# Optimization experiments

Measured on AMD Instinct MI355X. Metric: run time of the kernel, lower is better.

The kernel has to match this reference:

```python
import jax, jax.numpy as jnp
import numpy as np

D_MODEL = 1024
HEADDIM = 64
EXPAND = 2
D_STATE = 128
D_CONV = 4
NGROUPS = 1
D_INNER = EXPAND * D_MODEL            # 2048
NHEADS = D_INNER // HEADDIM           # 32
CONV_DIM = D_INNER + 2 * NGROUPS * D_STATE
D_IN_PROJ = 2 * D_INNER + 2 * NGROUPS * D_STATE + NHEADS
BATCH = 2
SEQLEN = 1024
EPS = 1e-5


def silu(v):
    return v * jax.nn.sigmoid(v)


def setup_inputs() -> dict:
    key = jax.random.key(0)
    ks = jax.random.split(key, 8)
    s = 0.02
    return {
        "x": jax.random.normal(ks[0], (BATCH, SEQLEN, D_MODEL), jnp.float32),
        "in_proj_w": jax.random.normal(ks[1], (D_IN_PROJ, D_MODEL), jnp.float32) * s,
        "conv_w": jax.random.normal(ks[2], (CONV_DIM, D_CONV), jnp.float32) * 0.2,
        "conv_b": jax.random.normal(ks[3], (CONV_DIM,), jnp.float32) * 0.02,
        "dt_bias": jax.random.normal(ks[4], (NHEADS,), jnp.float32) * 0.1,
        "A_log": jax.random.normal(ks[5], (NHEADS,), jnp.float32) * 0.5,
        "D": jax.random.normal(ks[6], (NHEADS,), jnp.float32) * 0.5,
        "norm_w": jnp.ones((D_INNER,), jnp.float32),
        "out_proj_w": jax.random.normal(ks[7], (D_MODEL, D_INNER), jnp.float32) * s,
    }


def _mamba2(x, in_proj_w, conv_w, conv_b, dt_bias, A_log, D, norm_w, out_proj_w):
    b, l, _ = x.shape
    # input projection -> z | xBC | dt
    zxbcdt = x @ in_proj_w.T                                  # [b,l,d_in_proj]
    z, xBC, dt = jnp.split(zxbcdt, [D_INNER, D_INNER + CONV_DIM], axis=-1)
    dt = jax.nn.softplus(dt + dt_bias)                        # [b,l,nh]
    # causal depthwise conv over time, then SiLU
    rhs = conv_w.T[:, None, :]                                # [d_conv, 1, conv_dim]
    xBC = jax.lax.conv_general_dilated(
        xBC, rhs, window_strides=(1,), padding=[(D_CONV - 1, 0)],
        dimension_numbers=("NWC", "WIO", "NWC"), feature_group_count=CONV_DIM)
    xBC = silu(xBC + conv_b)
    xs, Bm, Cm = jnp.split(xBC, [D_INNER, D_INNER + D_STATE], axis=-1)
    xs = xs.reshape(b, l, NHEADS, HEADDIM)                    # [b,l,h,p]
    A = -jnp.exp(A_log)                                       # [nh], negative
    dA = jnp.exp(dt * A)                                      # [b,l,nh] in (0,1)
    # selective scan: h_t = dA_t * h_{t-1} + dt_t * x_t (outer) B_t; y_t = h_t C_t
    def step(h, inp):
        dA_t, x_t, B_t, dt_t, C_t = inp                       # [b,h],[b,h,p],[b,n],[b,h],[b,n]
        h = h * dA_t[:, :, None, None] + jnp.einsum("bh,bhp,bn->bhpn", dt_t, x_t, B_t)
        y = jnp.einsum("bhpn,bn->bhp", h, C_t)
        return h, y

    h0 = jnp.zeros((b, NHEADS, HEADDIM, D_STATE), x.dtype)
    xs_t = xs.transpose(1, 0, 2, 3)
    _, ys = jax.lax.scan(step, h0, (dA.transpose(1, 0, 2), xs_t,
                                    Bm.transpose(1, 0, 2), dt.transpose(1, 0, 2),
                                    Cm.transpose(1, 0, 2)))
    y = ys.transpose(1, 0, 2, 3) + D[None, None, :, None] * xs  # skip term
    y = y.reshape(b, l, D_INNER)
    # gated RMSNorm (norm_before_gate=False): rmsnorm(y * silu(z)) * w
    y = y * silu(z)
    y = y * jax.lax.rsqrt(jnp.mean(y * y, axis=-1, keepdims=True) + EPS) * norm_w
    return y @ out_proj_w.T


def reference(x, in_proj_w, conv_w, conv_b, dt_bias, A_log, D, norm_w, out_proj_w):
    return x + _mamba2(x, in_proj_w, conv_w, conv_b, dt_bias, A_log, D, norm_w, out_proj_w)
```

## Files before the change

kernel.cpp:

```cpp
#include <hip/hip_runtime.h>
#include <hip/hip_bf16.h>
#include <math.h>

#define NHEADS   32
#define CONV_DIM 2304
#define D_INNER  2048
#define SEQLEN   1024
#define NROWS    2048
#define ZX_STR   4352
#define D_MODEL  1024
#define Q        64
#define NCHUNK   16
#define XT_STR   72

typedef __attribute__((ext_vector_type(8))) short bhalf8;
typedef __attribute__((ext_vector_type(8))) short short8;
typedef __attribute__((ext_vector_type(4))) short short4v;
typedef __attribute__((ext_vector_type(4))) float f32x4;

__device__ __forceinline__ float bf2f(__hip_bfloat16 v){ return __bfloat162float(v); }
__device__ __forceinline__ short f2bs(float f){ __hip_bfloat16 h = __float2bfloat16(f); return *(short*)&h; }
__device__ __forceinline__ float s2f(short s){ __hip_bfloat16 h = *(__hip_bfloat16*)&s; return __bfloat162float(h); }
__device__ __forceinline__ float rdin(const void* p, size_t i, int isf){
    return isf ? ((const float*)p)[i] : __bfloat162float(((const __hip_bfloat16*)p)[i]);
}

__global__ __launch_bounds__(256)
void detect_dtype(const unsigned short* __restrict__ p, int* __restrict__ flag)
{
    int cnt = 0;
    for (int i = threadIdx.x; i < 4096; i += 256) {
        unsigned short u = p[2 * i];
        int e = (u >> 7) & 0xFF;
        cnt += (e >= 90 && e <= 141) ? 1 : 0;
    }
#pragma unroll
    for (int m = 1; m < 64; m <<= 1) cnt += __shfl_xor(cnt, m);
    __shared__ int red[4];
    if ((threadIdx.x & 63) == 0) red[threadIdx.x >> 6] = cnt;
    __syncthreads();
    if (threadIdx.x == 0) *flag = ((red[0]+red[1]+red[2]+red[3]) < 2048) ? 1 : 0;
}

#define XN8 262144
#define WN8 561152
#define ON8 262144
__global__ __launch_bounds__(256)
void to_bf16_all(const void* __restrict__ xs, const void* __restrict__ ws,
                 const void* __restrict__ os,
                 __hip_bfloat16* __restrict__ xd, __hip_bfloat16* __restrict__ wd,
                 __hip_bfloat16* __restrict__ od, const int* __restrict__ flagp)
{
    const int isf = *flagp;
    int i = blockIdx.x * 256 + threadIdx.x;
    const void* src; __hip_bfloat16* dst; int j;
    if (i < XN8)            { src = xs; dst = xd; j = i; }
    else if (i < XN8 + WN8) { src = ws; dst = wd; j = i - XN8; }
    else                    { src = os; dst = od; j = i - XN8 - WN8; }
    if (isf) {
        const float4* s = (const float4*)src;
        float4 a = s[2 * j], b = s[2 * j + 1];
        short8 r;
        r[0]=f2bs(a.x); r[1]=f2bs(a.y); r[2]=f2bs(a.z); r[3]=f2bs(a.w);
        r[4]=f2bs(b.x); r[5]=f2bs(b.y); r[6]=f2bs(b.z); r[7]=f2bs(b.w);
        ((short8*)dst)[j] = r;
    } else {
        ((float4*)dst)[j] = ((const float4*)src)[j];
    }
}

template<int MODE, int MT, int NT, int WROWS, int WCOLS>
__global__ __launch_bounds__(256)
void gemm_bt(const __hip_bfloat16* __restrict__ A,
             const __hip_bfloat16* __restrict__ W,
             __hip_bfloat16* __restrict__ Cb,
             const void* __restrict__ xraw,
             void* __restrict__ outv,
             const int* __restrict__ flagp,
             int K, int N)
{
    constexpr int FM = MT / WROWS / 16;
    constexpr int FN = NT / WCOLS / 16;
    constexpr int AI = MT / 32;
    constexpr int BI = NT / 32;
    __shared__ short As[MT * 64];
    __shared__ short Bs[NT * 64];
    const int m0 = blockIdx.y * MT;
    const int n0 = blockIdx.x * NT;
    const int wave = threadIdx.x >> 6;
    const int lane = threadIdx.x & 63;
    const int lr8 = lane >> 3, lc8 = lane & 7;
    const int lr  = lane & 15, lq  = lane >> 4;
    const int wm = (wave / WCOLS) * (MT / WROWS);
    const int wn = (wave % WCOLS) * (NT / WCOLS);

    f32x4 acc[FM][FN];
#pragma unroll
    for (int i = 0; i < FM; ++i)
#pragma unroll
        for (int j = 0; j < FN; ++j) acc[i][j] = (f32x4){0.f,0.f,0.f,0.f};

    for (int k0 = 0; k0 < K; k0 += 64) {
#pragma unroll
        for (int i = 0; i < AI; ++i) {
            const int rt = (wave * AI + i) * 8;
            const __hip_bfloat16* gp = A + (size_t)(m0 + rt + lr8) * K + k0 + lc8 * 8;
            __builtin_amdgcn_global_load_lds(
                (const __attribute__((address_space(1))) void*)gp,
                (__attribute__((address_space(3))) void*)&As[rt * 64], 16, 0, 0);
        }
#pragma unroll
        for (int i = 0; i < BI; ++i) {
            const int rt = (wave * BI + i) * 8;
            const __hip_bfloat16* gp = W + (size_t)(n0 + rt + lr8) * K + k0 + lc8 * 8;
            __builtin_amdgcn_global_load_lds(
                (const __attribute__((address_space(1))) void*)gp,
                (__attribute__((address_space(3))) void*)&Bs[rt * 64], 16, 0, 0);
        }
        __syncthreads();
#pragma unroll
        for (int kk = 0; kk < 64; kk += 32) {
            bhalf8 af[FM], bfv[FN];
#pragma unroll
            for (int t = 0; t < FM; ++t)
                af[t]  = *(const bhalf8*)&As[(wm + t * 16 + lr) * 64 + kk + lq * 8];
#pragma unroll
            for (int t = 0; t < FN; ++t)
                bfv[t] = *(const bhalf8*)&Bs[(wn + t * 16 + lr) * 64 + kk + lq * 8];
#pragma unroll
            for (int ti = 0; ti < FM; ++ti)
#pragma unroll
                for (int tj = 0; tj < FN; ++tj)
                    acc[ti][tj] = __builtin_amdgcn_mfma_f32_16x16x32_bf16(
                        af[ti], bfv[tj], acc[ti][tj], 0, 0, 0);
        }
        __syncthreads();
    }

    const int isf = (MODE == 1) ? *flagp : 0;
#pragma unroll
    for (int ti = 0; ti < FM; ++ti)
#pragma unroll
        for (int tj = 0; tj < FN; ++tj)
#pragma unroll
            for (int r = 0; r < 4; ++r) {
                int m = m0 + wm + ti * 16 + lq * 4 + r;
                int n = n0 + wn + tj * 16 + lr;
                size_t idx = (size_t)m * N + n;
                float v = acc[ti][tj][r];
                if (MODE == 0) {
                    Cb[idx] = __float2bfloat16(v);
                } else {
                    v += rdin(xraw, idx, isf);
                    if (isf) ((float*)outv)[idx] = v;
                    else     ((__hip_bfloat16*)outv)[idx] = __float2bfloat16(v);
                }
            }
}

__global__ __launch_bounds__(256)
void dt_kernel(const void* __restrict__ xraw, const void* __restrict__ wraw,
               const void* __restrict__ dt_bias,
               const int* __restrict__ flagp,
               float* __restrict__ dtp)
{
    const int isf = *flagp;
    const int row = blockIdx.x;
    __shared__ float xs[D_MODEL];
    for (int k = threadIdx.x; k < D_MODEL; k += 256)
        xs[k] = rdin(xraw, (size_t)row * D_MODEL + k, isf);
    __syncthreads();
    const int h = threadIdx.x >> 3;
    const int t = threadIdx.x & 7;
    const size_t wbase = (size_t)(4352 + h) * D_MODEL;
    float s = 0.f;
    for (int k = t; k < D_MODEL; k += 8)
        s += xs[k] * rdin(wraw, wbase + k, isf);
    s += __shfl_xor(s, 1);
    s += __shfl_xor(s, 2);
    s += __shfl_xor(s, 4);
    if (t == 0) {
        float raw = s + rdin(dt_bias, h, isf);
        dtp[(size_t)row * NHEADS + h] = raw > 20.f ? raw : log1pf(expf(raw));
    }
}

__global__ __launch_bounds__(256)
void conv_silu(const __hip_bfloat16* __restrict__ zxb,
               const void* __restrict__ conv_w, const void* __restrict__ conv_b,
               const int* __restrict__ flagp,
               __hip_bfloat16* __restrict__ xs_bf,
               __hip_bfloat16* __restrict__ B_bf,
               __hip_bfloat16* __restrict__ C_bf)
{
    const int isf = *flagp;
    const int row = blockIdx.x;
    const int l = row & (SEQLEN - 1);
    for (int c = threadIdx.x; c < CONV_DIM; c += 256) {
        float acc = rdin(conv_b, c, isf);
#pragma unroll
        for (int j = 0; j < 4; ++j) {
            int ls = l - 3 + j;
            if (ls >= 0)
                acc += bf2f(zxb[(size_t)(row - 3 + j) * ZX_STR + 2048 + c]) *
                       rdin(conv_w, (size_t)c * 4 + j, isf);
        }
        float v = acc / (1.f + expf(-acc));
        __hip_bfloat16 bv = __float2bfloat16(v);
        if (c < 2048)       xs_bf[(size_t)row * 2048 + c] = bv;
        else if (c < 2176)  B_bf[(size_t)row * 128 + (c - 2048)] = bv;
        else                C_bf[(size_t)row * 128 + (c - 2176)] = bv;
    }
}

__global__ __launch_bounds__(256)
void chunk_kernel(const __hip_bfloat16* __restrict__ xs_bf,
                  const __hip_bfloat16* __restrict__ B_bf,
                  const __hip_bfloat16* __restrict__ C_bf,
                  const float* __restrict__ dtp, const void* __restrict__ Alog,
                  const int* __restrict__ flagp,
                  float* __restrict__ cumg, float* __restrict__ decayg,
                  __hip_bfloat16* __restrict__ M_bf, float* __restrict__ S)
{
    __shared__ float cumS[Q], uS[Q], dtS[Q];
    __shared__ short Xt[64 * XT_STR];
    __shared__ short Bt[128 * XT_STR];
    const int bhc = blockIdx.x;
    const int c = bhc & 15, h = (bhc >> 4) & 31, b = bhc >> 9;
    const int row0 = b * SEQLEN + c * Q;
    const int isf = *flagp;

    if (threadIdx.x < 64) {
        const int t = threadIdx.x;
        const float An = -expf(rdin(Alog, h, isf));
        const float dt = dtp[(size_t)(row0 + t) * NHEADS + h];
        float cum = dt * An;
#pragma unroll
        for (int ofs = 1; ofs < 64; ofs <<= 1) {
            float v = __shfl_up(cum, ofs);
            if (t >= ofs) cum += v;
        }
        float tot = __shfl(cum, 63);
        cumS[t] = cum; dtS[t] = dt;
        uS[t] = expf(tot - cum) * dt;
        cumg[(size_t)bhc * Q + t] = cum;
        if (t == 63) decayg[bhc] = expf(tot);
    }
    __syncthreads();

#pragma unroll
    for (int i = 0; i < 2; ++i) {
        int seg = threadIdx.x + i * 256;
        int t = seg >> 3, p8 = (seg & 7) * 8;
        float ut = uS[t];
        bhalf8 v = *(const bhalf8*)&xs_bf[(size_t)(row0 + t) * 2048 + h * 64 + p8];
#pragma unroll
        for (int j = 0; j < 8; ++j)
            Xt[(p8 + j) * XT_STR + t] = f2bs(s2f(v[j]) * ut);
    }
#pragma unroll
    for (int i = 0; i < 4; ++i) {
        int seg = threadIdx.x + i * 256;
        int t = seg >> 4, n8 = (seg & 15) * 8;
        bhalf8 v = *(const bhalf8*)&B_bf[(size_t)(row0 + t) * 128 + n8];
#pragma unroll
        for (int j = 0; j < 8; ++j)
            Bt[(n8 + j) * XT_STR + t] = v[j];
    }

    const int wave = threadIdx.x >> 6, lane = threadIdx.x & 63;
    const int lr = lane & 15, lq = lane >> 4;

    {
        const int t0 = wave * 16;
        f32x4 acc[4];
#pragma unroll
        for (int j = 0; j < 4; ++j) acc[j] = (f32x4){0.f,0.f,0.f,0.f};
#pragma unroll
        for (int kk = 0; kk < 128; kk += 32) {
            bhalf8 af = *(const bhalf8*)&C_bf[(size_t)(row0 + t0 + lr) * 128 + kk + lq * 8];
#pragma unroll
            for (int j = 0; j < 4; ++j) {
                bhalf8 bf = *(const bhalf8*)&B_bf[(size_t)(row0 + j * 16 + lr) * 128 + kk + lq * 8];
                acc[j] = __builtin_amdgcn_mfma_f32_16x16x32_bf16(af, bf, acc[j], 0, 0, 0);
            }
        }
#pragma unroll
        for (int j = 0; j < 4; ++j)
#pragma unroll
            for (int r = 0; r < 4; ++r) {
                int t = t0 + lq * 4 + r;
                int s = j * 16 + lr;
                float m = (s <= t) ? acc[j][r] * expf(cumS[t] - cumS[s]) * dtS[s] : 0.f;
                M_bf[(size_t)bhc * 4096 + t * 64 + s] = __float2bfloat16(m);
            }
    }
    __syncthreads();

    {
        const int p0 = wave * 16;
        f32x4 acc[8];
#pragma unroll
        for (int j = 0; j < 8; ++j) acc[j] = (f32x4){0.f,0.f,0.f,0.f};
#pragma unroll
        for (int kk = 0; kk < 64; kk += 32) {
            bhalf8 af = *(const bhalf8*)&Xt[(p0 + lr) * XT_STR + kk + lq * 8];
#pragma unroll
            for (int j = 0; j < 8; ++j) {
                bhalf8 bf = *(const bhalf8*)&Bt[(j * 16 + lr) * XT_STR + kk + lq * 8];
                acc[j] = __builtin_amdgcn_mfma_f32_16x16x32_bf16(af, bf, acc[j], 0, 0, 0);
            }
        }
#pragma unroll
        for (int j = 0; j < 8; ++j)
#pragma unroll
            for (int r = 0; r < 4; ++r) {
                int p = p0 + lq * 4 + r;
                int n = j * 16 + lr;
                S[(size_t)bhc * 8192 + p * 128 + n] = acc[j][r];
            }
    }
}

__global__ __launch_bounds__(256)
void rec_kernel(const float* __restrict__ S, const float* __restrict__ decayg,
                __hip_bfloat16* __restrict__ hst)
{
    const int bh = blockIdx.x >> 3;
    const int sl = blockIdx.x & 7;
    const int off = sl * 1024 + threadIdx.x * 4;
    float h0 = 0.f, h1 = 0.f, h2 = 0.f, h3 = 0.f;
    for (int c = 0; c < NCHUNK; ++c) {
        size_t base = ((size_t)bh * NCHUNK + c) * 8192 + off;
        short4v hb;
        hb[0] = f2bs(h0); hb[1] = f2bs(h1); hb[2] = f2bs(h2); hb[3] = f2bs(h3);
        *(short4v*)&hst[base] = hb;
        float4 s = *(const float4*)&S[base];
        float d = decayg[bh * NCHUNK + c];
        h0 = fmaf(h0, d, s.x); h1 = fmaf(h1, d, s.y);
        h2 = fmaf(h2, d, s.z); h3 = fmaf(h3, d, s.w);
    }
}

__global__ __launch_bounds__(256)
void y_kernel(const __hip_bfloat16* __restrict__ M_bf,
              const __hip_bfloat16* __restrict__ xs_bf,
              const __hip_bfloat16* __restrict__ C_bf,
              const __hip_bfloat16* __restrict__ hst,
              const float* __restrict__ cumg,
              const void* __restrict__ Draw, const int* __restrict__ flagp,
              float* __restrict__ yws)
{
    __shared__ short Xt[64 * XT_STR];
    const int bhc = blockIdx.x;
    const int c = bhc & 15, h = (bhc >> 4) & 31, b = bhc >> 9;
    const int row0 = b * SEQLEN + c * Q;
    const int isf = *flagp;
    const float Dh = rdin(Draw, h, isf);

#pragma unroll
    for (int i = 0; i < 2; ++i) {
        int seg = threadIdx.x + i * 256;
        int t = seg >> 3, p8 = (seg & 7) * 8;
        bhalf8 v = *(const bhalf8*)&xs_bf[(size_t)(row0 + t) * 2048 + h * 64 + p8];
#pragma unroll
        for (int j = 0; j < 8; ++j)
            Xt[(p8 + j) * XT_STR + t] = v[j];
    }
    __syncthreads();

    const int wave = threadIdx.x >> 6, lane = threadIdx.x & 63;
    const int lr = lane & 15, lq = lane >> 4;
    const int t0 = wave * 16;
    f32x4 acc1[4], acc2[4];
#pragma unroll
    for (int j = 0; j < 4; ++j) { acc1[j] = (f32x4){0.f,0.f,0.f,0.f}; acc2[j] = acc1[j]; }

#pragma unroll
    for (int kk = 0; kk < 64; kk += 32) {
        bhalf8 af = *(const bhalf8*)&M_bf[(size_t)bhc * 4096 + (t0 + lr) * 64 + kk + lq * 8];
#pragma unroll
        for (int j = 0; j < 4; ++j) {
            bhalf8 bf = *(const bhalf8*)&Xt[(j * 16 + lr) * XT_STR + kk + lq * 8];
            acc1[j] = __builtin_amdgcn_mfma_f32_16x16x32_bf16(af, bf, acc1[j], 0, 0, 0);
        }
    }
#pragma unroll
    for (int kk = 0; kk < 128; kk += 32) {
        bhalf8 af = *(const bhalf8*)&C_bf[(size_t)(row0 + t0 + lr) * 128 + kk + lq * 8];
#pragma unroll
        for (int j = 0; j < 4; ++j) {
            bhalf8 bf = *(const bhalf8*)&hst[(size_t)bhc * 8192 + (j * 16 + lr) * 128 + kk + lq * 8];
            acc2[j] = __builtin_amdgcn_mfma_f32_16x16x32_bf16(af, bf, acc2[j], 0, 0, 0);
        }
    }
    float ex[4];
#pragma unroll
    for (int r = 0; r < 4; ++r) ex[r] = expf(cumg[(size_t)bhc * Q + t0 + lq * 4 + r]);
#pragma unroll
    for (int j = 0; j < 4; ++j)
#pragma unroll
        for (int r = 0; r < 4; ++r) {
            int t = t0 + lq * 4 + r;
            int p = j * 16 + lr;
            float xv = s2f(Xt[p * XT_STR + t]);
            float y = acc1[j][r] + ex[r] * acc2[j][r] + Dh * xv;
            yws[(size_t)(row0 + t) * D_INNER + h * 64 + p] = y;
        }
}

__global__ __launch_bounds__(256)
void gate_norm(const float* __restrict__ yws,
               const __hip_bfloat16* __restrict__ zxb,
               const void* __restrict__ norm_w,
               const int* __restrict__ flagp,
               __hip_bfloat16* __restrict__ yg)
{
    const int isf = *flagp;
    const int row = blockIdx.x;
    const float* y = yws + (size_t)row * D_INNER;
    const __hip_bfloat16* z = zxb + (size_t)row * ZX_STR;
    float v[8]; float ss = 0.f;
#pragma unroll
    for (int it = 0; it < 8; ++it) {
        int c = it * 256 + threadIdx.x;
        float zz = bf2f(z[c]);
        float vv = y[c] * (zz / (1.f + expf(-zz)));
        v[it] = vv;
        ss += vv * vv;
    }
#pragma unroll
    for (int m = 1; m < 64; m <<= 1) ss += __shfl_xor(ss, m);
    __shared__ float red[4];
    if ((threadIdx.x & 63) == 0) red[threadIdx.x >> 6] = ss;
    __syncthreads();
    float tot = red[0] + red[1] + red[2] + red[3];
    float scale = rsqrtf(tot / (float)D_INNER + 1e-5f);
#pragma unroll
    for (int it = 0; it < 8; ++it) {
        int c = it * 256 + threadIdx.x;
        yg[(size_t)row * D_INNER + c] =
            __float2bfloat16(v[it] * scale * rdin(norm_w, c, isf));
    }
}

extern "C" void kernel_launch(void* const* d_in, const int* in_sizes, int n_in,
                              void* d_out, int out_size, void* d_ws, size_t ws_size,
                              hipStream_t stream)
{
    const void* x_raw    = d_in[0];
    const void* inw_raw  = d_in[1];
    const void* convw    = d_in[2];
    const void* convb    = d_in[3];
    const void* dtb      = d_in[4];
    const void* Alog     = d_in[5];
    const void* Dsk      = d_in[6];
    const void* normw    = d_in[7];
    const void* outw_raw = d_in[8];

    char* ws = (char*)d_ws;
    size_t off = 0;
    int* flag = (int*)(ws + off);                      off += 256;
    __hip_bfloat16* xb    = (__hip_bfloat16*)(ws+off); off += (size_t)NROWS * D_MODEL * 2;
    __hip_bfloat16* inwb  = (__hip_bfloat16*)(ws+off); off += (size_t)4384 * D_MODEL * 2;
    __hip_bfloat16* outwb = (__hip_bfloat16*)(ws+off); off += (size_t)D_MODEL * D_INNER * 2;
    __hip_bfloat16* zxb   = (__hip_bfloat16*)(ws+off); off += (size_t)NROWS * ZX_STR * 2;
    __hip_bfloat16* xs_bf = (__hip_bfloat16*)(ws+off); off += (size_t)NROWS * 2048 * 2;
    __hip_bfloat16* B_bf  = (__hip_bfloat16*)(ws+off); off += (size_t)NROWS * 128 * 2;
    __hip_bfloat16* C_bf  = (__hip_bfloat16*)(ws+off); off += (size_t)NROWS * 128 * 2;
    float* dtp   = (float*)(ws+off);                   off += (size_t)NROWS * NHEADS * 4;
    float* cumg  = (float*)(ws+off);                   off += (size_t)1024 * Q * 4;
    float* decayg= (float*)(ws+off);                   off += (size_t)1024 * 4;
    __hip_bfloat16* M_bf  = (__hip_bfloat16*)(ws+off); off += (size_t)1024 * 4096 * 2;
    __hip_bfloat16* hst   = (__hip_bfloat16*)(ws+off); off += (size_t)1024 * 8192 * 2;
    float* S = (float*)(ws+off);                       off += (size_t)1024 * 8192 * 4;
    float* yws = S;
    __hip_bfloat16* yg = (__hip_bfloat16*)(S + (size_t)NROWS * D_INNER);

    detect_dtype<<<1, 256, 0, stream>>>((const unsigned short*)x_raw, flag);
    to_bf16_all<<<(XN8+WN8+ON8)/256, 256, 0, stream>>>(x_raw, inw_raw, outw_raw,
                                                       xb, inwb, outwb, flag);
    gemm_bt<0,64,128,1,4><<<dim3(34, 32), 256, 0, stream>>>(
        xb, inwb, zxb, nullptr, nullptr, flag, D_MODEL, ZX_STR);
    dt_kernel<<<NROWS, 256, 0, stream>>>(x_raw, inw_raw, dtb, flag, dtp);
    conv_silu<<<NROWS, 256, 0, stream>>>(zxb, convw, convb, flag, xs_bf, B_bf, C_bf);
    chunk_kernel<<<1024, 256, 0, stream>>>(xs_bf, B_bf, C_bf, dtp, Alog, flag,
                                           cumg, decayg, M_bf, S);
    rec_kernel<<<512, 256, 0, stream>>>(S, decayg, hst);
    y_kernel<<<1024, 256, 0, stream>>>(M_bf, xs_bf, C_bf, hst, cumg, Dsk, flag, yws);
    gate_norm<<<NROWS, 256, 0, stream>>>(yws, zxb, normw, flag, yg);
    gemm_bt<1,64,64,2,2><<<dim3(16, 32), 256, 0, stream>>>(
        yg, outwb, nullptr, x_raw, d_out, flag, D_INNER, D_MODEL);
}
```

Baseline: 265.3 us.

## Swizzle GEMM LDS layout and batch 8 rows in dt and conv kernels

The GEMM loads its tiles into LDS with an XOR swizzle on the 16-byte column segment, keyed by row, to remove bank conflicts on the MFMA fragment reads. The dt projection kernel now handles 8 rows per block, so each weight load is reused across 8 rows. The conv+SiLU kernel stages an 11-row window of the conv input in LDS and computes 8 output rows per block, loading conv weights once per channel. Both kernels launch far fewer blocks (256 instead of 2048), which reduces parallelism, and conv_silu needs about 50KB of LDS per block, which may limit occupancy.

```diff
diff --git a/kernel.cpp b/kernel.cpp
--- a/kernel.cpp
+++ b/kernel.cpp
@@ -93,6 +93,7 @@
     const int lr  = lane & 15, lq  = lane >> 4;
     const int wm = (wave / WCOLS) * (MT / WROWS);
     const int wn = (wave % WCOLS) * (NT / WCOLS);
+    const int swl = lr & 7;
 
     f32x4 acc[FM][FN];
 #pragma unroll
@@ -104,7 +105,7 @@
 #pragma unroll
         for (int i = 0; i < AI; ++i) {
             const int rt = (wave * AI + i) * 8;
-            const __hip_bfloat16* gp = A + (size_t)(m0 + rt + lr8) * K + k0 + lc8 * 8;
+            const __hip_bfloat16* gp = A + (size_t)(m0 + rt + lr8) * K + k0 + ((lc8 ^ lr8) << 3);
             __builtin_amdgcn_global_load_lds(
                 (const __attribute__((address_space(1))) void*)gp,
                 (__attribute__((address_space(3))) void*)&As[rt * 64], 16, 0, 0);
@@ -112,7 +113,7 @@
 #pragma unroll
         for (int i = 0; i < BI; ++i) {
             const int rt = (wave * BI + i) * 8;
-            const __hip_bfloat16* gp = W + (size_t)(n0 + rt + lr8) * K + k0 + lc8 * 8;
+            const __hip_bfloat16* gp = W + (size_t)(n0 + rt + lr8) * K + k0 + ((lc8 ^ lr8) << 3);
             __builtin_amdgcn_global_load_lds(
                 (const __attribute__((address_space(1))) void*)gp,
                 (__attribute__((address_space(3))) void*)&Bs[rt * 64], 16, 0, 0);
@@ -120,13 +121,14 @@
         __syncthreads();
 #pragma unroll
         for (int kk = 0; kk < 64; kk += 32) {
+            const int sw = (((kk >> 3) + lq) ^ swl) << 3;
             bhalf8 af[FM], bfv[FN];
 #pragma unroll
             for (int t = 0; t < FM; ++t)
-                af[t]  = *(const bhalf8*)&As[(wm + t * 16 + lr) * 64 + kk + lq * 8];
+                af[t]  = *(const bhalf8*)&As[(wm + t * 16 + lr) * 64 + sw];
 #pragma unroll
             for (int t = 0; t < FN; ++t)
-                bfv[t] = *(const bhalf8*)&Bs[(wn + t * 16 + lr) * 64 + kk + lq * 8];
+                bfv[t] = *(const bhalf8*)&Bs[(wn + t * 16 + lr) * 64 + sw];
 #pragma unroll
             for (int ti = 0; ti < FM; ++ti)
 #pragma unroll
@@ -165,23 +167,35 @@
                float* __restrict__ dtp)
 {
     const int isf = *flagp;
-    const int row = blockIdx.x;
-    __shared__ float xs[D_MODEL];
-    for (int k = threadIdx.x; k < D_MODEL; k += 256)
-        xs[k] = rdin(xraw, (size_t)row * D_MODEL + k, isf);
+    const int r0 = blockIdx.x * 8;
+    __shared__ float xs[8][D_MODEL];
+    for (int idx = threadIdx.x; idx < 8 * D_MODEL; idx += 256)
+        ((float*)xs)[idx] = rdin(xraw, (size_t)r0 * D_MODEL + idx, isf);
     __syncthreads();
     const int h = threadIdx.x >> 3;
     const int t = threadIdx.x & 7;
     const size_t wbase = (size_t)(4352 + h) * D_MODEL;
-    float s = 0.f;
-    for (int k = t; k < D_MODEL; k += 8)
-        s += xs[k] * rdin(wraw, wbase + k, isf);
-    s += __shfl_xor(s, 1);
-    s += __shfl_xor(s, 2);
-    s += __shfl_xor(s, 4);
+    float s[8];
+#pragma unroll
+    for (int r = 0; r < 8; ++r) s[r] = 0.f;
+    for (int k = t; k < D_MODEL; k += 8) {
+        float wv = rdin(wraw, wbase + k, isf);
+#pragma unroll
+        for (int r = 0; r < 8; ++r) s[r] = fmaf(xs[r][k], wv, s[r]);
+    }
+#pragma unroll
+    for (int r = 0; r < 8; ++r) {
+        s[r] += __shfl_xor(s[r], 1);
+        s[r] += __shfl_xor(s[r], 2);
+        s[r] += __shfl_xor(s[r], 4);
+    }
     if (t == 0) {
-        float raw = s + rdin(dt_bias, h, isf);
-        dtp[(size_t)row * NHEADS + h] = raw > 20.f ? raw : log1pf(expf(raw));
+        float bias = rdin(dt_bias, h, isf);
+#pragma unroll
+        for (int r = 0; r < 8; ++r) {
+            float raw = s[r] + bias;
+            dtp[(size_t)(r0 + r) * NHEADS + h] = raw > 20.f ? raw : log1pf(expf(raw));
+        }
     }
 }
 
@@ -193,23 +207,47 @@
                __hip_bfloat16* __restrict__ B_bf,
                __hip_bfloat16* __restrict__ C_bf)
 {
+    __shared__ short buf[11 * CONV_DIM];
     const int isf = *flagp;
-    const int row = blockIdx.x;
-    const int l = row & (SEQLEN - 1);
-    for (int c = threadIdx.x; c < CONV_DIM; c += 256) {
-        float acc = rdin(conv_b, c, isf);
-#pragma unroll
-        for (int j = 0; j < 4; ++j) {
-            int ls = l - 3 + j;
-            if (ls >= 0)
-                acc += bf2f(zxb[(size_t)(row - 3 + j) * ZX_STR + 2048 + c]) *
-                       rdin(conv_w, (size_t)c * 4 + j, isf);
-        }
-        float v = acc / (1.f + expf(-acc));
-        __hip_bfloat16 bv = __float2bfloat16(v);
-        if (c < 2048)       xs_bf[(size_t)row * 2048 + c] = bv;
-        else if (c < 2176)  B_bf[(size_t)row * 128 + (c - 2048)] = bv;
-        else                C_bf[(size_t)row * 128 + (c - 2176)] = bv;
+    const int r0 = blockIdx.x * 8;
+    const int bstart = r0 & ~(SEQLEN - 1);
+    for (int idx = threadIdx.x; idx < 11 * (CONV_DIM / 8); idx += 256) {
+        int ii = idx / (CONV_DIM / 8);
+        int seg = idx % (CONV_DIM / 8);
+        int g = r0 - 3 + ii;
+        bhalf8 v;
+        if (g >= bstart) {
+            v = *(const bhalf8*)&zxb[(size_t)g * ZX_STR + 2048 + seg * 8];
+        } else {
+#pragma unroll
+            for (int j = 0; j < 8; ++j) v[j] = 0;
+        }
+        *(bhalf8*)&buf[ii * CONV_DIM + seg * 8] = v;
+    }
+    __syncthreads();
+
+#pragma unroll
+    for (int j = 0; j < CONV_DIM / 256; ++j) {
+        const int c = threadIdx.x + j * 256;
+        float w0 = rdin(conv_w, (size_t)c * 4 + 0, isf);
+        float w1 = rdin(conv_w, (size_t)c * 4 + 1, isf);
+        float w2 = rdin(conv_w, (size_t)c * 4 + 2, isf);
+        float w3 = rdin(conv_w, (size_t)c * 4 + 3, isf);
+        float bias = rdin(conv_b, c, isf);
+#pragma unroll
+        for (int r = 0; r < 8; ++r) {
+            float acc = bias;
+            acc = fmaf(s2f(buf[(r + 0) * CONV_DIM + c]), w0, acc);
+            acc = fmaf(s2f(buf[(r + 1) * CONV_DIM + c]), w1, acc);
+            acc = fmaf(s2f(buf[(r + 2) * CONV_DIM + c]), w2, acc);
+            acc = fmaf(s2f(buf[(r + 3) * CONV_DIM + c]), w3, acc);
+            float v = acc / (1.f + expf(-acc));
+            __hip_bfloat16 bv = __float2bfloat16(v);
+            int row = r0 + r;
+            if (c < 2048)       xs_bf[(size_t)row * 2048 + c] = bv;
+            else if (c < 2176)  B_bf[(size_t)row * 128 + (c - 2048)] = bv;
+            else                C_bf[(size_t)row * 128 + (c - 2176)] = bv;
+        }
     }
 }
 
@@ -482,8 +520,8 @@
                                                        xb, inwb, outwb, flag);
     gemm_bt<0,64,128,1,4><<<dim3(34, 32), 256, 0, stream>>>(
         xb, inwb, zxb, nullptr, nullptr, flag, D_MODEL, ZX_STR);
-    dt_kernel<<<NROWS, 256, 0, stream>>>(x_raw, inw_raw, dtb, flag, dtp);
-    conv_silu<<<NROWS, 256, 0, stream>>>(zxb, convw, convb, flag, xs_bf, B_bf, C_bf);
+    dt_kernel<<<256, 256, 0, stream>>>(x_raw, inw_raw, dtb, flag, dtp);
+    conv_silu<<<256, 256, 0, stream>>>(zxb, convw, convb, flag, xs_bf, B_bf, C_bf);
     chunk_kernel<<<1024, 256, 0, stream>>>(xs_bf, B_bf, C_bf, dtp, Alog, flag,
                                            cumg, decayg, M_bf, S);
     rec_kernel<<<512, 256, 0, stream>>>(S, decayg, hst);
```

New measurement: 256.7 us. -3.2%, faster.
